# Kernel optimization log

Measured on AMD Instinct MI355X. Metric: run time of the kernel, lower is better.

Reference implementation:

```python
import jax, jax.numpy as jnp
import numpy as np

BS, N_PTS, N_SAMPLES = 8, 8192, 2048
GRID_SIZE = 4096
MAX_X, MAX_Y, MAX_Z = 25.0, 25.0, 5.0
P_NORM = 1


def _sample_axis(key, max_v):
    # linspace(-max_v, max_v, GRID_SIZE) indexed by multinomial(uniform, replacement=False)
    rng = jnp.linspace(-max_v, max_v, GRID_SIZE, dtype=jnp.float32)
    idx = jax.random.choice(key, GRID_SIZE, (N_SAMPLES,), replace=False)
    return rng[idx]


def setup_inputs() -> dict:
    key = jax.random.key(0)
    k1, k2, kx, ky, kz = jax.random.split(key, 5)
    gts = jax.random.normal(k1, (BS, N_PTS, 3), dtype=jnp.float32) * 10.0
    preds = jax.random.normal(k2, (BS, N_PTS, 3), dtype=jnp.float32) * 10.0
    gx = _sample_axis(kx, MAX_X)
    gy = _sample_axis(ky, MAX_Y)
    gz = _sample_axis(kz, MAX_Z)
    grid = jnp.stack([gx, gy, gz], axis=1)  # (N_SAMPLES, 3)
    grid_points = jnp.broadcast_to(grid[None], (BS, N_SAMPLES, 3)).astype(jnp.float32)
    return {"gts": gts, "preds": preds, "grid_points": grid_points}


def _cdist(x, y):
    # Euclidean cdist: (b, n, d) x (b, m, d) -> (b, n, m)
    x2 = jnp.sum(x * x, axis=-1)[:, :, None]
    y2 = jnp.sum(y * y, axis=-1)[:, None, :]
    xy = jnp.einsum('bnd,bmd->bnm', x, y)
    return jnp.sqrt(jnp.maximum(x2 + y2 - 2.0 * xy, 0.0))


def reference(gts, preds, grid_points):
    mins = jnp.min(_cdist(grid_points, preds), axis=2)   # (b, n_samples)
    mins2 = jnp.min(_cdist(grid_points, gts), axis=2)    # (b, n_samples)
    diff = jnp.abs(mins - mins2)
    if P_NORM == 2:
        diff = diff ** 2
    return jnp.mean(diff, axis=1)  # (b,)
```

## Files before the change

kernel.cpp:

```cpp
#include <hip/hip_runtime.h>
#include <math.h>

#define BS 8
#define N_PTS 8192
#define N_SAMPLES 2048
#define THREADS 256
#define SPT 8
#define PSPLIT 128
#define CHUNK (N_PTS / PSPLIT)

__global__ __launch_bounds__(THREADS, 1)
void chamfer_min_kernel(const float* __restrict__ gts,
                        const float* __restrict__ preds,
                        const float* __restrict__ grid,
                        unsigned int* __restrict__ wsmin)
{
    const int bid = blockIdx.x;
    const int b   = bid >> 7;
    const int pc  = bid & (PSPLIT - 1);
    const int t   = threadIdx.x;

    __shared__ float4 ldsP[CHUNK];
    __shared__ float4 ldsG[CHUNK];

    if (t < 2 * CHUNK) {
        const int j = t & (CHUNK - 1);
        const float* src = ((t < CHUNK) ? preds : gts)
                         + ((size_t)b * N_PTS + (size_t)pc * CHUNK + j) * 3;
        const float x = src[0], y = src[1], z = src[2];
        const float4 v = make_float4(x, y, z, fmaf(x, x, fmaf(y, y, z * z)));
        if (t < CHUNK) ldsP[j] = v; else ldsG[j] = v;
    }

    float nsx[SPT], nsy[SPT], nsz[SPT], mP[SPT], mG[SPT];
    {
        const float* grow = grid + (size_t)b * N_SAMPLES * 3;
#pragma unroll
        for (int k = 0; k < SPT; ++k) {
            const int s = k * THREADS + t;
            nsx[k] = -2.0f * grow[s * 3 + 0];
            nsy[k] = -2.0f * grow[s * 3 + 1];
            nsz[k] = -2.0f * grow[s * 3 + 2];
            mP[k] = 3.0e38f;
            mG[k] = 3.0e38f;
        }
    }

    __syncthreads();

#pragma unroll 2
    for (int j = 0; j < CHUNK; j += 2) {
        const float4 p0 = ldsP[j], p1 = ldsP[j + 1];
        const float4 g0 = ldsG[j], g1 = ldsG[j + 1];
#pragma unroll
        for (int k = 0; k < SPT; ++k) {
            const float x = nsx[k], y = nsy[k], z = nsz[k];
            const float t0 = fmaf(p0.x, x, fmaf(p0.y, y, fmaf(p0.z, z, p0.w)));
            const float t1 = fmaf(p1.x, x, fmaf(p1.y, y, fmaf(p1.z, z, p1.w)));
            mP[k] = fminf(fminf(t0, t1), mP[k]);
            const float u0 = fmaf(g0.x, x, fmaf(g0.y, y, fmaf(g0.z, z, g0.w)));
            const float u1 = fmaf(g1.x, x, fmaf(g1.y, y, fmaf(g1.z, z, g1.w)));
            mG[k] = fminf(fminf(u0, u1), mG[k]);
        }
    }

    unsigned int* wp = wsmin + (size_t)b * N_SAMPLES;
    unsigned int* wg = wsmin + (size_t)(BS + b) * N_SAMPLES;
#pragma unroll
    for (int k = 0; k < SPT; ++k) {
        const int s = k * THREADS + t;
        const float s2 = 0.25f * fmaf(nsx[k], nsx[k], fmaf(nsy[k], nsy[k], nsz[k] * nsz[k]));
        atomicMin(&wp[s], __float_as_uint(fmaxf(mP[k] + s2, 0.0f)));
        atomicMin(&wg[s], __float_as_uint(fmaxf(mG[k] + s2, 0.0f)));
    }
}

__global__ __launch_bounds__(THREADS)
void chamfer_finish_kernel(const unsigned int* __restrict__ wsmin,
                           float* __restrict__ out)
{
    const int b = blockIdx.x;
    const int t = threadIdx.x;
    const unsigned int* wp = wsmin + (size_t)b * N_SAMPLES;
    const unsigned int* wg = wsmin + (size_t)(BS + b) * N_SAMPLES;

    float sum = 0.0f;
#pragma unroll
    for (int s = t; s < N_SAMPLES; s += THREADS) {
        const float dp = sqrtf(__uint_as_float(wp[s]));
        const float dg = sqrtf(__uint_as_float(wg[s]));
        sum += fabsf(dp - dg);
    }

#pragma unroll
    for (int off = 32; off > 0; off >>= 1)
        sum += __shfl_down(sum, off, 64);

    __shared__ float wsum[THREADS / 64];
    const int wid = t >> 6;
    if ((t & 63) == 0) wsum[wid] = sum;
    __syncthreads();
    if (t == 0) {
        float tot = 0.0f;
#pragma unroll
        for (int w = 0; w < THREADS / 64; ++w) tot += wsum[w];
        out[b] = tot / (float)N_SAMPLES;
    }
}

extern "C" void kernel_launch(void* const* d_in, const int* in_sizes, int n_in,
                              void* d_out, int out_size, void* d_ws, size_t ws_size,
                              hipStream_t stream)
{
    const float* gts   = (const float*)d_in[0];
    const float* preds = (const float*)d_in[1];
    const float* grid  = (const float*)d_in[2];
    float* out = (float*)d_out;
    unsigned int* wsmin = (unsigned int*)d_ws;

    const size_t wsbytes = (size_t)2 * BS * N_SAMPLES * sizeof(unsigned int);
    hipMemsetAsync(d_ws, 0x7F, wsbytes, stream);

    chamfer_min_kernel<<<dim3(BS * PSPLIT), dim3(THREADS), 0, stream>>>(gts, preds, grid, wsmin);
    chamfer_finish_kernel<<<dim3(BS), dim3(THREADS), 0, stream>>>(wsmin, out);
}
```

Baseline: 35.71 us.

## Compute min-distance dot products with split-fp16 MFMA instead of scalar FMA

Adds a prep kernel that packs points and grid samples into fp16 hi/lo split operands, so that a 32x32x16 fp16 MFMA computes -2*s·p + |p|^2 at near-fp32 accuracy. The main kernel then reduces the MFMA accumulators with min, combines partial minima in LDS with atomics, and writes them to global memory using an order-preserving float encoding so negative values are handled. The memset is replaced by initialisation inside the prep kernel, and |s|^2 is added in the finish kernel. In exchange it adds an extra launch plus packing traffic, and the hi/lo fp16 split carries some precision risk.

```diff
diff --git a/kernel.cpp b/kernel.cpp
--- a/kernel.cpp
+++ b/kernel.cpp
@@ -4,91 +4,181 @@
 #define BS 8
 #define N_PTS 8192
 #define N_SAMPLES 2048
-#define THREADS 256
-#define SPT 8
-#define PSPLIT 128
-#define CHUNK (N_PTS / PSPLIT)
-
-__global__ __launch_bounds__(THREADS, 1)
-void chamfer_min_kernel(const float* __restrict__ gts,
-                        const float* __restrict__ preds,
-                        const float* __restrict__ grid,
-                        unsigned int* __restrict__ wsmin)
-{
+
+#define APACK_F4 (2 * BS * 256 * 64)
+#define BPACK_F4 (BS * 64 * 64)
+#define S2_F     (BS * N_SAMPLES)
+#define WSMIN_U  (2 * BS * N_SAMPLES)
+
+typedef float f32x16 __attribute__((ext_vector_type(16)));
+typedef _Float16 half8 __attribute__((ext_vector_type(8)));
+
+union H8 { _Float16 h[8]; float4 f4; };
+
+__device__ inline unsigned encf(float x) {
+    unsigned u = __float_as_uint(x);
+    return (u & 0x80000000u) ? ~u : (u | 0x80000000u);
+}
+__device__ inline float decf(unsigned u) {
+    unsigned b = (u & 0x80000000u) ? (u ^ 0x80000000u) : ~u;
+    return __uint_as_float(b);
+}
+
+__global__ __launch_bounds__(256)
+void chamfer_prep_kernel(const float* __restrict__ gts,
+                         const float* __restrict__ preds,
+                         const float* __restrict__ grid,
+                         float4* __restrict__ apack,
+                         float4* __restrict__ bpack,
+                         float* __restrict__ s2f,
+                         unsigned* __restrict__ wsmin)
+{
+    const int tid = blockIdx.x * 256 + threadIdx.x;
+
+    {
+        const int sd = tid >> 17;
+        const int b  = (tid >> 14) & 7;
+        const int st = (tid >> 6) & 255;
+        const int l  = tid & 63;
+        const int g  = l >> 5;
+        const int idx = st * 32 + (l & 31);
+        const float* src = sd ? gts : preds;
+        const float x = src[((size_t)b * N_PTS + idx) * 3 + 0];
+        const float y = src[((size_t)b * N_PTS + idx) * 3 + 1];
+        const float z = src[((size_t)b * N_PTS + idx) * 3 + 2];
+        const _Float16 hx = (_Float16)x, hy = (_Float16)y, hz = (_Float16)z;
+        const _Float16 lx = (_Float16)(x - (float)hx);
+        const _Float16 ly = (_Float16)(y - (float)hy);
+        const _Float16 lz = (_Float16)(z - (float)hz);
+        const float hp = fmaf(x, x, fmaf(y, y, z * z));
+        const _Float16 hh = (_Float16)hp;
+        const _Float16 hl = (_Float16)(hp - (float)hh);
+        H8 u;
+        if (g == 0) {
+            u.h[0] = hx; u.h[1] = hy; u.h[2] = hz;
+            u.h[3] = hx; u.h[4] = hy; u.h[5] = hz;
+            u.h[6] = lx; u.h[7] = ly;
+        } else {
+            u.h[0] = lz; u.h[1] = hh; u.h[2] = hl;
+            u.h[3] = (_Float16)0.f; u.h[4] = (_Float16)0.f;
+            u.h[5] = (_Float16)0.f; u.h[6] = (_Float16)0.f; u.h[7] = (_Float16)0.f;
+        }
+        apack[tid] = u.f4;
+    }
+
+    if (tid < BPACK_F4) {
+        const int b    = tid >> 12;
+        const int tile = (tid >> 6) & 63;
+        const int l    = tid & 63;
+        const int g    = l >> 5;
+        const int s    = tile * 32 + (l & 31);
+        const float nx = -2.0f * grid[((size_t)b * N_SAMPLES + s) * 3 + 0];
+        const float ny = -2.0f * grid[((size_t)b * N_SAMPLES + s) * 3 + 1];
+        const float nz = -2.0f * grid[((size_t)b * N_SAMPLES + s) * 3 + 2];
+        const _Float16 nhx = (_Float16)nx, nhy = (_Float16)ny, nhz = (_Float16)nz;
+        const _Float16 nlx = (_Float16)(nx - (float)nhx);
+        const _Float16 nly = (_Float16)(ny - (float)nhy);
+        const _Float16 nlz = (_Float16)(nz - (float)nhz);
+        H8 u;
+        if (g == 0) {
+            u.h[0] = nhx; u.h[1] = nhy; u.h[2] = nhz;
+            u.h[3] = nlx; u.h[4] = nly; u.h[5] = nlz;
+            u.h[6] = nhx; u.h[7] = nhy;
+        } else {
+            u.h[0] = nhz; u.h[1] = (_Float16)1.0f; u.h[2] = (_Float16)1.0f;
+            u.h[3] = (_Float16)0.f; u.h[4] = (_Float16)0.f;
+            u.h[5] = (_Float16)0.f; u.h[6] = (_Float16)0.f; u.h[7] = (_Float16)0.f;
+        }
+        bpack[tid] = u.f4;
+    }
+
+    if (tid < S2_F) {
+        const int b = tid >> 11;
+        const int s = tid & 2047;
+        const float x = grid[((size_t)b * N_SAMPLES + s) * 3 + 0];
+        const float y = grid[((size_t)b * N_SAMPLES + s) * 3 + 1];
+        const float z = grid[((size_t)b * N_SAMPLES + s) * 3 + 2];
+        s2f[tid] = fmaf(x, x, fmaf(y, y, z * z));
+    }
+
+    if (tid < WSMIN_U) wsmin[tid] = 0xFFFFFFFFu;
+}
+
+__device__ inline float rmin16(const f32x16& v) {
+    const float a = fminf(fminf(v[0], v[1]), fminf(v[2], v[3]));
+    const float b = fminf(fminf(v[4], v[5]), fminf(v[6], v[7]));
+    const float c = fminf(fminf(v[8], v[9]), fminf(v[10], v[11]));
+    const float d = fminf(fminf(v[12], v[13]), fminf(v[14], v[15]));
+    return fminf(fminf(a, b), fminf(c, d));
+}
+
+__global__ __launch_bounds__(256, 1)
+void chamfer_mfma_kernel(const float4* __restrict__ apack,
+                         const float4* __restrict__ bpack,
+                         unsigned* __restrict__ wsmin)
+{
+    __shared__ float4 bstage[2048];
+    __shared__ unsigned minbuf[1024];
+
     const int bid = blockIdx.x;
     const int b   = bid >> 7;
-    const int pc  = bid & (PSPLIT - 1);
+    const int sd  = (bid >> 6) & 1;
+    const int grp = (bid >> 1) & 31;
+    const int h   = bid & 1;
     const int t   = threadIdx.x;
 
-    __shared__ float4 ldsP[CHUNK];
-    __shared__ float4 ldsG[CHUNK];
-
-    if (t < 2 * CHUNK) {
-        const int j = t & (CHUNK - 1);
-        const float* src = ((t < CHUNK) ? preds : gts)
-                         + ((size_t)b * N_PTS + (size_t)pc * CHUNK + j) * 3;
-        const float x = src[0], y = src[1], z = src[2];
-        const float4 v = make_float4(x, y, z, fmaf(x, x, fmaf(y, y, z * z)));
-        if (t < CHUNK) ldsP[j] = v; else ldsG[j] = v;
-    }
-
-    float nsx[SPT], nsy[SPT], nsz[SPT], mP[SPT], mG[SPT];
-    {
-        const float* grow = grid + (size_t)b * N_SAMPLES * 3;
-#pragma unroll
-        for (int k = 0; k < SPT; ++k) {
-            const int s = k * THREADS + t;
-            nsx[k] = -2.0f * grow[s * 3 + 0];
-            nsy[k] = -2.0f * grow[s * 3 + 1];
-            nsz[k] = -2.0f * grow[s * 3 + 2];
-            mP[k] = 3.0e38f;
-            mG[k] = 3.0e38f;
-        }
-    }
-
+    const float4* bsrc = bpack + ((size_t)b * 64 + h * 32) * 64;
+#pragma unroll
+    for (int i = 0; i < 8; ++i) bstage[i * 256 + t] = bsrc[i * 256 + t];
+#pragma unroll
+    for (int i = 0; i < 4; ++i) minbuf[i * 256 + t] = 0xFFFFFFFFu;
     __syncthreads();
 
+    const int w = t >> 6, l = t & 63;
+    const int st0 = grp * 8 + w * 2;
+    const float4* abase = apack + (((size_t)sd * BS + b) * 256) * 64;
+    union { float4 f4; half8 v; } ra0, ra1, rb;
+    ra0.f4 = abase[(size_t)st0 * 64 + l];
+    ra1.f4 = abase[(size_t)(st0 + 1) * 64 + l];
+
+    const f32x16 zacc = (f32x16)(0.0f);
+
 #pragma unroll 2
-    for (int j = 0; j < CHUNK; j += 2) {
-        const float4 p0 = ldsP[j], p1 = ldsP[j + 1];
-        const float4 g0 = ldsG[j], g1 = ldsG[j + 1];
-#pragma unroll
-        for (int k = 0; k < SPT; ++k) {
-            const float x = nsx[k], y = nsy[k], z = nsz[k];
-            const float t0 = fmaf(p0.x, x, fmaf(p0.y, y, fmaf(p0.z, z, p0.w)));
-            const float t1 = fmaf(p1.x, x, fmaf(p1.y, y, fmaf(p1.z, z, p1.w)));
-            mP[k] = fminf(fminf(t0, t1), mP[k]);
-            const float u0 = fmaf(g0.x, x, fmaf(g0.y, y, fmaf(g0.z, z, g0.w)));
-            const float u1 = fmaf(g1.x, x, fmaf(g1.y, y, fmaf(g1.z, z, g1.w)));
-            mG[k] = fminf(fminf(u0, u1), mG[k]);
-        }
-    }
-
-    unsigned int* wp = wsmin + (size_t)b * N_SAMPLES;
-    unsigned int* wg = wsmin + (size_t)(BS + b) * N_SAMPLES;
-#pragma unroll
-    for (int k = 0; k < SPT; ++k) {
-        const int s = k * THREADS + t;
-        const float s2 = 0.25f * fmaf(nsx[k], nsx[k], fmaf(nsy[k], nsy[k], nsz[k] * nsz[k]));
-        atomicMin(&wp[s], __float_as_uint(fmaxf(mP[k] + s2, 0.0f)));
-        atomicMin(&wg[s], __float_as_uint(fmaxf(mG[k] + s2, 0.0f)));
-    }
-}
-
-__global__ __launch_bounds__(THREADS)
-void chamfer_finish_kernel(const unsigned int* __restrict__ wsmin,
+    for (int tt = 0; tt < 32; ++tt) {
+        rb.f4 = bstage[tt * 64 + l];
+        const f32x16 d0 = __builtin_amdgcn_mfma_f32_32x32x16_f16(ra0.v, rb.v, zacc, 0, 0, 0);
+        const f32x16 d1 = __builtin_amdgcn_mfma_f32_32x32x16_f16(ra1.v, rb.v, zacc, 0, 0, 0);
+        float m = fminf(rmin16(d0), rmin16(d1));
+        m = fminf(m, __shfl_xor(m, 32, 64));
+        if (l < 32) atomicMin(&minbuf[tt * 32 + l], encf(m));
+    }
+
+    __syncthreads();
+    unsigned* wdst = wsmin + ((size_t)sd * BS + b) * N_SAMPLES + h * 1024;
+#pragma unroll
+    for (int i = 0; i < 4; ++i) {
+        const int ls = i * 256 + t;
+        atomicMin(&wdst[ls], minbuf[ls]);
+    }
+}
+
+__global__ __launch_bounds__(256)
+void chamfer_finish_kernel(const unsigned* __restrict__ wsmin,
+                           const float* __restrict__ s2f,
                            float* __restrict__ out)
 {
     const int b = blockIdx.x;
     const int t = threadIdx.x;
-    const unsigned int* wp = wsmin + (size_t)b * N_SAMPLES;
-    const unsigned int* wg = wsmin + (size_t)(BS + b) * N_SAMPLES;
 
     float sum = 0.0f;
 #pragma unroll
-    for (int s = t; s < N_SAMPLES; s += THREADS) {
-        const float dp = sqrtf(__uint_as_float(wp[s]));
-        const float dg = sqrtf(__uint_as_float(wg[s]));
+    for (int i = 0; i < 8; ++i) {
+        const int s = i * 256 + t;
+        const float s2 = s2f[(size_t)b * N_SAMPLES + s];
+        const float fp = decf(wsmin[(size_t)b * N_SAMPLES + s]) + s2;
+        const float fg = decf(wsmin[((size_t)BS + b) * N_SAMPLES + s]) + s2;
+        const float dp = sqrtf(fmaxf(fp, 0.0f));
+        const float dg = sqrtf(fmaxf(fg, 0.0f));
         sum += fabsf(dp - dg);
     }
 
@@ -96,16 +186,11 @@
     for (int off = 32; off > 0; off >>= 1)
         sum += __shfl_down(sum, off, 64);
 
-    __shared__ float wsum[THREADS / 64];
-    const int wid = t >> 6;
-    if ((t & 63) == 0) wsum[wid] = sum;
+    __shared__ float wsum[4];
+    if ((t & 63) == 0) wsum[t >> 6] = sum;
     __syncthreads();
-    if (t == 0) {
-        float tot = 0.0f;
-#pragma unroll
-        for (int w = 0; w < THREADS / 64; ++w) tot += wsum[w];
-        out[b] = tot / (float)N_SAMPLES;
-    }
+    if (t == 0)
+        out[b] = ((wsum[0] + wsum[1]) + (wsum[2] + wsum[3])) / (float)N_SAMPLES;
 }
 
 extern "C" void kernel_launch(void* const* d_in, const int* in_sizes, int n_in,
@@ -116,11 +201,14 @@
     const float* preds = (const float*)d_in[1];
     const float* grid  = (const float*)d_in[2];
     float* out = (float*)d_out;
-    unsigned int* wsmin = (unsigned int*)d_ws;
-
-    const size_t wsbytes = (size_t)2 * BS * N_SAMPLES * sizeof(unsigned int);
-    hipMemsetAsync(d_ws, 0x7F, wsbytes, stream);
-
-    chamfer_min_kernel<<<dim3(BS * PSPLIT), dim3(THREADS), 0, stream>>>(gts, preds, grid, wsmin);
-    chamfer_finish_kernel<<<dim3(BS), dim3(THREADS), 0, stream>>>(wsmin, out);
-}
+
+    float4* apack  = (float4*)d_ws;
+    float4* bpack  = apack + APACK_F4;
+    float*  s2f    = (float*)(bpack + BPACK_F4);
+    unsigned* wsmin = (unsigned*)(s2f + S2_F);
+
+    chamfer_prep_kernel<<<dim3(1024), dim3(256), 0, stream>>>(gts, preds, grid,
+                                                              apack, bpack, s2f, wsmin);
+    chamfer_mfma_kernel<<<dim3(1024), dim3(256), 0, stream>>>(apack, bpack, wsmin);
+    chamfer_finish_kernel<<<dim3(BS), dim3(256), 0, stream>>>(wsmin, s2f, out);
+}
```

Result: faster. 34.28 us (-4.0%).
